# Kernel optimization log

Hardware: AMD Instinct MI355X
Metric: run time of the kernel (lower is better)

Reference implementation:

```python
import jax, jax.numpy as jnp
import numpy as np


def setup_inputs() -> dict:
    key = jax.random.key(0)
    k1, k2, k3 = jax.random.split(key, 3)
    B, S, D, U = 256, 2048, 128, 64
    x = jax.random.normal(k1, (B, S, D), dtype=jnp.float32)
    # glorot-style scaling for the small projection weights
    W1 = jax.random.normal(k2, (D, U), dtype=jnp.float32) * (1.0 / np.sqrt(D))
    W2 = jax.random.normal(k3, (U, 1), dtype=jnp.float32) * (1.0 / np.sqrt(U))
    b = jnp.zeros((U,), dtype=jnp.float32)
    return {"x": x, "W1": W1, "W2": W2, "b": b}


def reference(x, W1, W2, b):
    # x: [B, S, D]; W1: [D, U]; W2: [U, 1]; b: [U]
    score = jnp.tanh(jnp.einsum("bsd,du->bsu", x, W1) + b)   # [B, S, U]
    score = jnp.einsum("bsu,uo->bso", score, W2)              # [B, S, 1]
    alpha = jax.nn.softmax(score, axis=1)                     # softmax over seq
    ctx = jnp.sum(x * alpha, axis=1)                          # [B, D]
    return (ctx, alpha)
```

## Files before the change

kernel.cpp:

```cpp
#include <hip/hip_runtime.h>
#include <math.h>

#define NB 256
#define NS 2048
#define ND 128
#define NU 64
#define NT 512
#define TS 128
#define NTILE (NS / TS)

typedef _Float16 f16x8 __attribute__((ext_vector_type(8)));
typedef float f32x4 __attribute__((ext_vector_type(4)));

#define GLDS16(gp, lp)                                                        \
  __builtin_amdgcn_global_load_lds(                                           \
      (const __attribute__((address_space(1))) void*)(gp),                    \
      (__attribute__((address_space(3))) void*)(lp), 16, 0, 0)

__device__ __forceinline__ float tanh_fast(float v) {
  const float e = __expf(2.0f * v);
  return 1.0f - 2.0f * __builtin_amdgcn_rcpf(e + 1.0f);
}

__global__ __launch_bounds__(NT, 2) void addattn_mfma(
    const float* __restrict__ x,
    const float* __restrict__ W1,
    const float* __restrict__ W2,
    const float* __restrict__ bias,
    float* __restrict__ out)
{
  __shared__ __align__(16) float xbuf[2][TS * ND];
  __shared__ float ps[NS];
  __shared__ __align__(16) float part[16][ND];
  __shared__ float red[8];

  const int b = blockIdx.x;
  const int t = threadIdx.x;
  const int lane = t & 63;
  const int wv = t >> 6;
  const int l15 = lane & 15;
  const int hi = lane >> 4;
  const float* xb = x + (size_t)b * NS * ND;

  f16x8 afrag[4][4];
#pragma unroll
  for (int mt = 0; mt < 4; ++mt) {
#pragma unroll
    for (int kt = 0; kt < 4; ++kt) {
      const int u = mt * 16 + l15;
      const int k0 = kt * 32 + hi * 8;
      f16x8 a;
#pragma unroll
      for (int j = 0; j < 8; ++j) a[j] = (_Float16)W1[(k0 + j) * NU + u];
      afrag[mt][kt] = a;
    }
  }
  float breg[4][4], wreg[4][4];
#pragma unroll
  for (int mt = 0; mt < 4; ++mt) {
#pragma unroll
    for (int r = 0; r < 4; ++r) {
      const int u = mt * 16 + hi * 4 + r;
      breg[mt][r] = bias[u];
      wreg[mt][r] = W2[u];
    }
  }

  auto stage = [&](int bi, int ti) {
    const float* src = xb + (size_t)ti * TS * ND;
    float* dst = &xbuf[bi][0];
#pragma unroll
    for (int j = 0; j < 8; ++j) {
      const int L = j * NT + t;
      const int s = L >> 5;
      const int d4 = (L & 31) ^ (s & 7);
      GLDS16(src + s * ND + d4 * 4, dst + L * 4);
    }
  };

  stage(0, 0);
  __syncthreads();

  f32x4 ctxa = {0.f, 0.f, 0.f, 0.f};
  const int srow = wv * 16 + l15;
  const int dq = t & 31;
  const int rbase = wv * 16 + ((lane >> 5) << 3);

  for (int ti = 0; ti < NTILE; ++ti) {
    const int cur = ti & 1;
    if (ti + 1 < NTILE) stage(cur ^ 1, ti + 1);
    const float* xl = &xbuf[cur][0];

    f32x4 acc[4];
#pragma unroll
    for (int mt = 0; mt < 4; ++mt) acc[mt] = (f32x4){0.f, 0.f, 0.f, 0.f};
    const int rb = srow * 32;
    const int sw = srow & 7;
#pragma unroll
    for (int kt = 0; kt < 4; ++kt) {
      const int d4a = kt * 8 + hi * 2;
      const float4 v0 = *(const float4*)(xl + (rb + ((d4a + 0) ^ sw)) * 4);
      const float4 v1 = *(const float4*)(xl + (rb + ((d4a + 1) ^ sw)) * 4);
      f16x8 bf;
      bf[0] = (_Float16)v0.x; bf[1] = (_Float16)v0.y;
      bf[2] = (_Float16)v0.z; bf[3] = (_Float16)v0.w;
      bf[4] = (_Float16)v1.x; bf[5] = (_Float16)v1.y;
      bf[6] = (_Float16)v1.z; bf[7] = (_Float16)v1.w;
#pragma unroll
      for (int mt = 0; mt < 4; ++mt)
        acc[mt] = __builtin_amdgcn_mfma_f32_16x16x32_f16(afrag[mt][kt], bf,
                                                         acc[mt], 0, 0, 0);
    }
    float s2 = 0.f;
#pragma unroll
    for (int mt = 0; mt < 4; ++mt) {
#pragma unroll
      for (int r = 0; r < 4; ++r)
        s2 = fmaf(tanh_fast(acc[mt][r] + breg[mt][r]), wreg[mt][r], s2);
    }
    s2 += __shfl_xor(s2, 16);
    s2 += __shfl_xor(s2, 32);
    const float p = __expf(s2);
    if (lane < 16) ps[ti * TS + srow] = p;

#pragma unroll
    for (int r8 = 0; r8 < 8; ++r8) {
      const int sr = rbase + r8;
      const float pv = __shfl(p, ((lane >> 5) << 3) + r8);
      const float4 xv = *(const float4*)(xl + (sr * 32 + (dq ^ (sr & 7))) * 4);
      ctxa[0] = fmaf(pv, xv.x, ctxa[0]);
      ctxa[1] = fmaf(pv, xv.y, ctxa[1]);
      ctxa[2] = fmaf(pv, xv.z, ctxa[2]);
      ctxa[3] = fmaf(pv, xv.w, ctxa[3]);
    }
    __syncthreads();
  }

  float lsum = 0.f;
#pragma unroll
  for (int j = 0; j < 4; ++j) lsum += ps[t + NT * j];
#pragma unroll
  for (int off = 32; off > 0; off >>= 1) lsum += __shfl_xor(lsum, off);
  if (lane == 0) red[wv] = lsum;
  *(float4*)(&part[t >> 5][dq * 4]) =
      make_float4(ctxa[0], ctxa[1], ctxa[2], ctxa[3]);
  __syncthreads();
  float l = 0.f;
#pragma unroll
  for (int j = 0; j < 8; ++j) l += red[j];
  const float inv = 1.0f / l;

  float* alpha_out = out + NB * ND;
#pragma unroll
  for (int j = 0; j < 4; ++j) {
    const int s = t + NT * j;
    alpha_out[(size_t)b * NS + s] = ps[s] * inv;
  }
  if (t < ND) {
    float sum = 0.f;
#pragma unroll
    for (int g = 0; g < 16; ++g) sum += part[g][t];
    out[(size_t)b * ND + t] = sum * inv;
  }
}

extern "C" void kernel_launch(void* const* d_in, const int* in_sizes, int n_in,
                              void* d_out, int out_size, void* d_ws,
                              size_t ws_size, hipStream_t stream) {
  const float* x = (const float*)d_in[0];
  const float* W1 = (const float*)d_in[1];
  const float* W2 = (const float*)d_in[2];
  const float* bias = (const float*)d_in[3];
  float* out = (float*)d_out;
  addattn_mfma<<<NB, NT, 0, stream>>>(x, W1, W2, bias, out);
}
```

Before: 52.81 us.

## Make each wave stage its own rows and drop per-tile block barriers

Each wave now loads only the 16 rows of each x tile that it consumes itself. This removes the per-iteration __syncthreads, and manual vmcnt waits replace the barrier. Prefetch is moved two tiles ahead, and the first tile load is issued before the W1 fragment setup so the load latency overlaps it. Without a barrier, waves drift independently, and correctness depends on the vmcnt counts matching the issued load count and on the LDS writes from global_load_lds being visible to the same wave after the wait.

```diff
diff --git a/kernel.cpp b/kernel.cpp
--- a/kernel.cpp
+++ b/kernel.cpp
@@ -42,6 +42,20 @@
   const int hi = lane >> 4;
   const float* xb = x + (size_t)b * NS * ND;
 
+  auto stage = [&](int bi, int ti) {
+    const float* src = xb + (size_t)ti * TS * ND + wv * 16 * ND;
+    float* dst = &xbuf[bi][wv * 16 * ND];
+#pragma unroll
+    for (int j = 0; j < 8; ++j) {
+      const int L = j * 64 + lane;
+      const int s = L >> 5;
+      const int d4 = (L & 31) ^ (s & 7);
+      GLDS16(src + s * ND + d4 * 4, dst + L * 4);
+    }
+  };
+
+  stage(0, 0);
+
   f16x8 afrag[4][4];
 #pragma unroll
   for (int mt = 0; mt < 4; ++mt) {
@@ -66,41 +80,32 @@
     }
   }
 
-  auto stage = [&](int bi, int ti) {
-    const float* src = xb + (size_t)ti * TS * ND;
-    float* dst = &xbuf[bi][0];
-#pragma unroll
-    for (int j = 0; j < 8; ++j) {
-      const int L = j * NT + t;
-      const int s = L >> 5;
-      const int d4 = (L & 31) ^ (s & 7);
-      GLDS16(src + s * ND + d4 * 4, dst + L * 4);
-    }
-  };
-
-  stage(0, 0);
-  __syncthreads();
+  stage(1, 1);
 
   f32x4 ctxa = {0.f, 0.f, 0.f, 0.f};
-  const int srow = wv * 16 + l15;
-  const int dq = t & 31;
-  const int rbase = wv * 16 + ((lane >> 5) << 3);
+  const int dq = lane & 31;
+  const int rloc = (lane >> 5) << 3;
 
   for (int ti = 0; ti < NTILE; ++ti) {
     const int cur = ti & 1;
-    if (ti + 1 < NTILE) stage(cur ^ 1, ti + 1);
-    const float* xl = &xbuf[cur][0];
+    if (ti < NTILE - 1) {
+      asm volatile("s_waitcnt vmcnt(8)" ::: "memory");
+    } else {
+      asm volatile("s_waitcnt vmcnt(0)" ::: "memory");
+    }
+    __builtin_amdgcn_sched_barrier(0);
+    const float* xs = &xbuf[cur][wv * 16 * ND];
 
     f32x4 acc[4];
 #pragma unroll
     for (int mt = 0; mt < 4; ++mt) acc[mt] = (f32x4){0.f, 0.f, 0.f, 0.f};
-    const int rb = srow * 32;
-    const int sw = srow & 7;
+    const int rb = l15 * 32;
+    const int sw = l15 & 7;
 #pragma unroll
     for (int kt = 0; kt < 4; ++kt) {
       const int d4a = kt * 8 + hi * 2;
-      const float4 v0 = *(const float4*)(xl + (rb + ((d4a + 0) ^ sw)) * 4);
-      const float4 v1 = *(const float4*)(xl + (rb + ((d4a + 1) ^ sw)) * 4);
+      const float4 v0 = *(const float4*)(xs + (rb + ((d4a + 0) ^ sw)) * 4);
+      const float4 v1 = *(const float4*)(xs + (rb + ((d4a + 1) ^ sw)) * 4);
       f16x8 bf;
       bf[0] = (_Float16)v0.x; bf[1] = (_Float16)v0.y;
       bf[2] = (_Float16)v0.z; bf[3] = (_Float16)v0.w;
@@ -121,20 +126,22 @@
     s2 += __shfl_xor(s2, 16);
     s2 += __shfl_xor(s2, 32);
     const float p = __expf(s2);
-    if (lane < 16) ps[ti * TS + srow] = p;
+    if (lane < 16) ps[ti * TS + wv * 16 + l15] = p;
 
 #pragma unroll
     for (int r8 = 0; r8 < 8; ++r8) {
-      const int sr = rbase + r8;
-      const float pv = __shfl(p, ((lane >> 5) << 3) + r8);
-      const float4 xv = *(const float4*)(xl + (sr * 32 + (dq ^ (sr & 7))) * 4);
+      const int sr = rloc + r8;
+      const float pv = __shfl(p, sr);
+      const float4 xv = *(const float4*)(xs + (sr * 32 + (dq ^ (sr & 7))) * 4);
       ctxa[0] = fmaf(pv, xv.x, ctxa[0]);
       ctxa[1] = fmaf(pv, xv.y, ctxa[1]);
       ctxa[2] = fmaf(pv, xv.z, ctxa[2]);
       ctxa[3] = fmaf(pv, xv.w, ctxa[3]);
     }
-    __syncthreads();
+
+    if (ti + 2 < NTILE) stage(cur, ti + 2);
   }
+  __syncthreads();
 
   float lsum = 0.f;
 #pragma unroll
```

After: 49.06 us, median of 2. -7.1%, faster.
